# Performance work log

Hardware: AMD Instinct MI355X
Metric: run time of the kernel (lower is better)

The kernel has to match this reference:

```python
import jax, jax.numpy as jnp
import numpy as np

N = 100000
F_IN = 128
H = 128
E = 1600000
EP = 200000


def _gcn_conv(x, W, b, src, dst, n):
    # GCNConv (PyG default): add self-loops done by caller; symmetric norm; linear + scatter-add.
    xw = x @ W                                        # [n, H]
    deg = jax.ops.segment_sum(jnp.ones(src.shape[0], x.dtype), dst, num_segments=n)
    dinv = jnp.where(deg > 0, jax.lax.rsqrt(deg), 0.0)
    norm = dinv[src] * dinv[dst]                      # [E']
    msg = xw[src] * norm[:, None]                     # [E', H] gather
    out = jax.ops.segment_sum(msg, dst, num_segments=n)  # scatter-add
    return out + b


def setup_inputs() -> dict:
    key = jax.random.key(0)
    k = jax.random.split(key, 9)
    x = jax.random.normal(k[0], (N, F_IN), dtype=jnp.float32)
    edge_index = jax.random.randint(k[1], (2, E), 0, N, dtype=jnp.int64)
    dict_node = jax.random.randint(k[2], (N,), 0, N, dtype=jnp.int64)
    pos_edge_index = jax.random.randint(k[3], (2, EP), 0, N, dtype=jnp.int64)
    neg_edge_index = jax.random.randint(k[4], (2, EP), 0, N, dtype=jnp.int64)
    s1 = 1.0 / np.sqrt(F_IN)
    s2 = 1.0 / np.sqrt(H)
    W1 = jax.random.uniform(k[5], (F_IN, H), jnp.float32, -s1, s1)
    b1 = jnp.zeros((H,), jnp.float32)
    W2 = jax.random.uniform(k[6], (H, H), jnp.float32, -s2, s2)
    b2 = jnp.zeros((H,), jnp.float32)
    return {"x": x, "W1": W1, "b1": b1, "W2": W2, "b2": b2,
            "edge_index": edge_index, "dict_node": dict_node,
            "pos_edge_index": pos_edge_index, "neg_edge_index": neg_edge_index}


def reference(x, W1, b1, W2, b2, edge_index, dict_node, pos_edge_index, neg_edge_index):
    n = x.shape[0]
    # add self-loops once (both convs use the same edge_index)
    loop = jnp.arange(n, dtype=edge_index.dtype)
    src = jnp.concatenate([edge_index[0], loop])
    dst = jnp.concatenate([edge_index[1], loop])
    # encode (dropout p=0.01 is identity in eval mode)
    h = jax.nn.relu(_gcn_conv(x, W1, b1, src, dst, n))
    h = jax.nn.relu(_gcn_conv(h, W2, b2, src, dst, n))
    # global_mean_pool over dict_node segments (size = num_nodes)
    sums = jax.ops.segment_sum(h, dict_node, num_segments=n)
    cnt = jax.ops.segment_sum(jnp.ones((n,), h.dtype), dict_node, num_segments=n)
    z = sums / jnp.maximum(cnt, 1.0)[:, None]
    # decode: per-edge dot products over concatenated pos/neg edges
    ei = jnp.concatenate([pos_edge_index, neg_edge_index], axis=-1)
    logits = jnp.sum(z[ei[0]] * z[ei[1]], axis=-1)
    return logits
```

## Files before the change

### kernel.cpp

```cpp
#include <hip/hip_runtime.h>
#include <hip/hip_fp16.h>

#define HH 128
#define PCHUNK 16384


__global__ __launch_bounds__(256) void part_count_k(const int* __restrict__ key, int e,
                                                    int nbkt, int nblk,
                                                    int* __restrict__ gcnt,
                                                    int* __restrict__ blkoff) {
  __shared__ int h[512];
  for (int i = threadIdx.x; i < nbkt; i += 256) h[i] = 0;
  __syncthreads();
  int start = blockIdx.x * PCHUNK;
  int cnt = e - start; if (cnt > PCHUNK) cnt = PCHUNK;
  for (int i = threadIdx.x; i < cnt; i += 256)
    atomicAdd(&h[key[start + i] >> 8], 1);
  __syncthreads();
  for (int i = threadIdx.x; i < nbkt; i += 256) {
    int c = h[i];
    if (c) blkoff[(size_t)i * nblk + blockIdx.x] = atomicAdd(&gcnt[i], c);
  }
}

__global__ __launch_bounds__(512) void scan_bkt_k(const int* __restrict__ gcnt,
                                                  int* __restrict__ bktbase, int nbkt, int e) {
  __shared__ int sc[512];
  int tid = threadIdx.x;
  int v = (tid < nbkt) ? gcnt[tid] : 0;
  sc[tid] = v;
  __syncthreads();
  for (int off = 1; off < 512; off <<= 1) {
    int t = (tid >= off) ? sc[tid - off] : 0;
    __syncthreads();
    sc[tid] += t;
    __syncthreads();
  }
  if (tid < nbkt) bktbase[tid] = sc[tid] - v;
  if (tid == 0) bktbase[nbkt] = e;
}

__global__ __launch_bounds__(256) void part_scatter_k(const int* __restrict__ src,
                                                      const int* __restrict__ key, int e,
                                                      int nbkt, int nblk,
                                                      const int* __restrict__ bktbase,
                                                      const int* __restrict__ blkoff,
                                                      int2* __restrict__ part) {
  __shared__ int cur[512];
  for (int i = threadIdx.x; i < nbkt; i += 256)
    cur[i] = bktbase[i] + blkoff[(size_t)i * nblk + blockIdx.x];
  __syncthreads();
  int start = blockIdx.x * PCHUNK;
  int cnt = e - start; if (cnt > PCHUNK) cnt = PCHUNK;
  for (int i = threadIdx.x; i < cnt; i += 256) {
    int d = key[start + i], s = src[start + i];
    int pos = atomicAdd(&cur[d >> 8], 1);
    part[pos] = make_int2(s, d);
  }
}

__global__ __launch_bounds__(256) void part_scatter_idx_k(const int* __restrict__ key, int e,
                                                          int nbkt, int nblk,
                                                          const int* __restrict__ bktbase,
                                                          const int* __restrict__ blkoff,
                                                          int2* __restrict__ part) {
  __shared__ int cur[512];
  for (int i = threadIdx.x; i < nbkt; i += 256)
    cur[i] = bktbase[i] + blkoff[(size_t)i * nblk + blockIdx.x];
  __syncthreads();
  int start = blockIdx.x * PCHUNK;
  int cnt = e - start; if (cnt > PCHUNK) cnt = PCHUNK;
  for (int i = threadIdx.x; i < cnt; i += 256) {
    int d = key[start + i];
    int pos = atomicAdd(&cur[d >> 8], 1);
    part[pos] = make_int2(start + i, d);
  }
}

__global__ __launch_bounds__(256) void bucket_csr_k(const int2* __restrict__ part,
                                                    const int* __restrict__ bktbase,
                                                    int* __restrict__ rowptr,
                                                    float* __restrict__ dinv,
                                                    int* __restrict__ esrc,
                                                    int n, int e, int nbkt) {
  __shared__ int hist[256];
  __shared__ int sc[256];
  __shared__ int cur[256];
  int tid = threadIdx.x;
  int b = blockIdx.x;
  int dstbase = b << 8;
  int nloc = n - dstbase; if (nloc > 256) nloc = 256;
  int beg = bktbase[b], bend = bktbase[b + 1];

  hist[tid] = 0;
  __syncthreads();
  for (int j = beg + tid; j < bend; j += 256)
    atomicAdd(&hist[part[j].y & 255], 1);
  __syncthreads();
  int v = hist[tid];
  sc[tid] = v;
  __syncthreads();
  for (int off = 1; off < 256; off <<= 1) {
    int t = (tid >= off) ? sc[tid - off] : 0;
    __syncthreads();
    sc[tid] += t;
    __syncthreads();
  }
  int excl = sc[tid] - v;
  if (tid < nloc) {
    rowptr[dstbase + tid] = beg + excl;
    cur[tid] = beg + excl;
    if (dinv) dinv[dstbase + tid] = rsqrtf((float)v + 1.0f);
  }
  __syncthreads();
  for (int j = beg + tid; j < bend; j += 256) {
    int2 p = part[j];
    int pos = atomicAdd(&cur[p.y & 255], 1);
    esrc[pos] = p.x;
  }
  if (b == nbkt - 1 && tid == 0) rowptr[n] = e;
}

template <bool OUT16>
__global__ __launch_bounds__(256) void gemm128_v4(const float* __restrict__ A,
                                                  const float* __restrict__ W,
                                                  const float* __restrict__ dscale,
                                                  void* __restrict__ out, int n) {
  __shared__ float As[64][65];
  const int tid = threadIdx.x;
  const int rbase = blockIdx.x * 64;
  const int vrows = (n - rbase) < 64 ? (n - rbase) : 64;

  const int r = tid & 63;
  const int q = __builtin_amdgcn_readfirstlane(tid >> 6);
  const float* Wq = W + q * 32;

  float4 acc[8];
  #pragma unroll
  for (int c = 0; c < 8; ++c) acc[c] = make_float4(0.f, 0.f, 0.f, 0.f);

  #pragma unroll
  for (int ph = 0; ph < 2; ++ph) {
    if (ph) __syncthreads();
    #pragma unroll
    for (int j = 0; j < 4; ++j) {
      int f = tid + 256 * j;
      int rr = f >> 4, c4 = f & 15;
      float4 v = (rr < vrows)
          ? ((const float4*)(A + (size_t)(rbase + rr) * HH + ph * 64))[c4]
          : make_float4(0.f, 0.f, 0.f, 0.f);
      As[rr][c4 * 4 + 0] = v.x;
      As[rr][c4 * 4 + 1] = v.y;
      As[rr][c4 * 4 + 2] = v.z;
      As[rr][c4 * 4 + 3] = v.w;
    }
    __syncthreads();

    #pragma unroll 4
    for (int kk = 0; kk < 64; ++kk) {
      float a = As[r][kk];
      const float4* Wr = (const float4*)(Wq + (size_t)(ph * 64 + kk) * HH);
      #pragma unroll
      for (int c = 0; c < 8; ++c) {
        float4 w = Wr[c];
        acc[c].x += a * w.x; acc[c].y += a * w.y;
        acc[c].z += a * w.z; acc[c].w += a * w.w;
      }
    }
  }

  int row = rbase + r;
  if (row < n) {
    float s = dscale ? dscale[row] : 1.0f;
    if (OUT16) {
      uint2* o = (uint2*)((__half*)out + (size_t)row * HH) + q * 8;
      #pragma unroll
      for (int c = 0; c < 8; ++c) {
        __half2 h0 = __float22half2_rn(make_float2(acc[c].x * s, acc[c].y * s));
        __half2 h1 = __float22half2_rn(make_float2(acc[c].z * s, acc[c].w * s));
        uint2 u;
        u.x = *reinterpret_cast<unsigned*>(&h0);
        u.y = *reinterpret_cast<unsigned*>(&h1);
        o[c] = u;
      }
    } else {
      float4* o = (float4*)((float*)out + (size_t)row * HH + q * 32);
      #pragma unroll
      for (int c = 0; c < 8; ++c) {
        acc[c].x *= s; acc[c].y *= s; acc[c].z *= s; acc[c].w *= s;
        o[c] = acc[c];
      }
    }
  }
}

__global__ __launch_bounds__(256) void gather16_k(const __half* __restrict__ xw16,
                                                  const int* __restrict__ rowptr,
                                                  const int* __restrict__ esrc,
                                                  const float* __restrict__ dinv,
                                                  const float* __restrict__ bias,
                                                  float* __restrict__ h, int n) {
  int wid = (int)((blockIdx.x * (size_t)blockDim.x + threadIdx.x) >> 6);
  int lane = threadIdx.x & 63;
  if (wid >= n) return;
  int beg = rowptr[wid], end = rowptr[wid + 1];
  int half = lane >> 5, l32 = lane & 31;
  const uint2* base = (const uint2*)xw16 + l32;
  float4 acc = make_float4(0.f, 0.f, 0.f, 0.f);

  for (int j0 = beg; j0 < end; j0 += 64) {
    int myj = j0 + lane;
    int sv = (myj < end) ? esrc[myj] : 0;
    int cnt = end - j0; if (cnt > 64) cnt = 64;
    int k = 0;
    for (; k + 8 <= cnt; k += 8) {
      #pragma unroll
      for (int p = 0; p < 4; ++p) {
        int sa = __builtin_amdgcn_readlane(sv, k + 2 * p);
        int sb = __builtin_amdgcn_readlane(sv, k + 2 * p + 1);
        unsigned off = (unsigned)(half ? sb : sa) << 5;
        uint2 u = base[off];
        float2 f0 = __half22float2(*reinterpret_cast<__half2*>(&u.x));
        float2 f1 = __half22float2(*reinterpret_cast<__half2*>(&u.y));
        acc.x += f0.x; acc.y += f0.y; acc.z += f1.x; acc.w += f1.y;
      }
    }
    for (; k + 2 <= cnt; k += 2) {
      int sa = __builtin_amdgcn_readlane(sv, k);
      int sb = __builtin_amdgcn_readlane(sv, k + 1);
      unsigned off = (unsigned)(half ? sb : sa) << 5;
      uint2 u = base[off];
      float2 f0 = __half22float2(*reinterpret_cast<__half2*>(&u.x));
      float2 f1 = __half22float2(*reinterpret_cast<__half2*>(&u.y));
      acc.x += f0.x; acc.y += f0.y; acc.z += f1.x; acc.w += f1.y;
    }
    if (k < cnt) {
      int sa = __builtin_amdgcn_readlane(sv, k);
      if (half == 0) {
        uint2 u = base[(unsigned)sa << 5];
        float2 f0 = __half22float2(*reinterpret_cast<__half2*>(&u.x));
        float2 f1 = __half22float2(*reinterpret_cast<__half2*>(&u.y));
        acc.x += f0.x; acc.y += f0.y; acc.z += f1.x; acc.w += f1.y;
      }
    }
  }
  acc.x += __shfl_xor(acc.x, 32);
  acc.y += __shfl_xor(acc.y, 32);
  acc.z += __shfl_xor(acc.z, 32);
  acc.w += __shfl_xor(acc.w, 32);
  if (half == 0) {
    uint2 u = base[(unsigned)wid << 5];
    float2 s0 = __half22float2(*reinterpret_cast<__half2*>(&u.x));
    float2 s1 = __half22float2(*reinterpret_cast<__half2*>(&u.y));
    float di = dinv[wid];
    float4 bb = ((const float4*)bias)[l32];
    float4 o;
    o.x = fmaxf(bb.x + di * (acc.x + s0.x), 0.f);
    o.y = fmaxf(bb.y + di * (acc.y + s0.y), 0.f);
    o.z = fmaxf(bb.z + di * (acc.z + s1.x), 0.f);
    o.w = fmaxf(bb.w + di * (acc.w + s1.y), 0.f);
    ((float4*)h)[((size_t)wid << 5) + l32] = o;
  }
}

__global__ __launch_bounds__(256) void decode_fused3_k(const float* __restrict__ h2,
                                                       const int* __restrict__ rowptr,
                                                       const int* __restrict__ nodelist,
                                                       const int* __restrict__ pos,
                                                       const int* __restrict__ neg,
                                                       float* __restrict__ out, int ep) {
  int wv = (int)((blockIdx.x * (size_t)blockDim.x + threadIdx.x) >> 6);
  int lane = threadIdx.x & 63;
  int qq = lane >> 4, l16 = lane & 15;
  int e0 = wv * 2;
  if (e0 >= 2 * ep) return;
  int edge = e0 + (qq >> 1);
  int side = qq & 1;
  bool live = edge < 2 * ep;
  int eL = live ? edge : 2 * ep - 1;
  int node;
  if (eL < ep) node = side ? pos[ep + eL] : pos[eL];
  else { int t = eL - ep; node = side ? neg[ep + t] : neg[t]; }

  int beg = rowptr[node], end = rowptr[node + 1];
  const float4* h4 = (const float4*)h2;
  float4 a0 = make_float4(0.f, 0.f, 0.f, 0.f);
  float4 a1 = make_float4(0.f, 0.f, 0.f, 0.f);
  float4 c0 = make_float4(0.f, 0.f, 0.f, 0.f);
  float4 c1 = make_float4(0.f, 0.f, 0.f, 0.f);

  for (int j = beg; j < end; j += 2) {
    bool two = (j + 1) < end;
    int m0 = nodelist[j];
    int m1 = two ? nodelist[j + 1] : m0;
    const float4* r0 = h4 + ((size_t)m0 << 5);
    const float4* r1 = h4 + ((size_t)m1 << 5);
    float4 u0 = r0[l16], u1 = r0[l16 + 16];
    float4 v0 = r1[l16], v1 = r1[l16 + 16];
    a0.x += u0.x; a0.y += u0.y; a0.z += u0.z; a0.w += u0.w;
    a1.x += u1.x; a1.y += u1.y; a1.z += u1.z; a1.w += u1.w;
    if (two) {
      c0.x += v0.x; c0.y += v0.y; c0.z += v0.z; c0.w += v0.w;
      c1.x += v1.x; c1.y += v1.y; c1.z += v1.z; c1.w += v1.w;
    }
  }
  a0.x += c0.x; a0.y += c0.y; a0.z += c0.z; a0.w += c0.w;
  a1.x += c1.x; a1.y += c1.y; a1.z += c1.z; a1.w += c1.w;

  float inv = 1.0f / fmaxf((float)(end - beg), 1.0f);
  a0.x *= inv; a0.y *= inv; a0.z *= inv; a0.w *= inv;
  a1.x *= inv; a1.y *= inv; a1.z *= inv; a1.w *= inv;

  float4 b0, b1;
  b0.x = __shfl_xor(a0.x, 16); b0.y = __shfl_xor(a0.y, 16);
  b0.z = __shfl_xor(a0.z, 16); b0.w = __shfl_xor(a0.w, 16);
  b1.x = __shfl_xor(a1.x, 16); b1.y = __shfl_xor(a1.y, 16);
  b1.z = __shfl_xor(a1.z, 16); b1.w = __shfl_xor(a1.w, 16);
  float p = a0.x * b0.x + a0.y * b0.y + a0.z * b0.z + a0.w * b0.w
          + a1.x * b1.x + a1.y * b1.y + a1.z * b1.z + a1.w * b1.w;
  #pragma unroll
  for (int off = 8; off > 0; off >>= 1) p += __shfl_xor(p, off);
  if (live && side == 0 && l16 == 0) out[edge] = p;
}

__global__ void fill_deg_k(float* __restrict__ deg, int n) {
  int i = blockIdx.x * blockDim.x + threadIdx.x;
  if (i < n) deg[i] = 1.0f;
}
__global__ void accum_deg_k(const int* __restrict__ dst, float* __restrict__ deg, int e) {
  int i = blockIdx.x * blockDim.x + threadIdx.x;
  if (i < e) atomicAdd(&deg[dst[i]], 1.0f);
}
__global__ void dinv_k(float* __restrict__ deg, int n) {
  int i = blockIdx.x * blockDim.x + threadIdx.x;
  if (i < n) deg[i] = rsqrtf(deg[i]);
}
__global__ void init_h_k(const float* __restrict__ xw, const float* __restrict__ bias,
                         const float* __restrict__ dinv, float* __restrict__ h, int n) {
  int gid = blockIdx.x * blockDim.x + threadIdx.x;
  int node = gid >> 5, c4 = gid & 31;
  if (node >= n) return;
  float di = dinv[node];
  float nm = di * di;
  float4 v = ((const float4*)(xw + (size_t)node * HH))[c4];
  float4 b = ((const float4*)bias)[c4];
  ((float4*)(h + (size_t)node * HH))[c4] =
      make_float4(b.x + nm * v.x, b.y + nm * v.y, b.z + nm * v.z, b.w + nm * v.w);
}
__global__ void scatter_k(const float* __restrict__ xw, float* __restrict__ h,
                          const float* __restrict__ dinv, const int* __restrict__ src,
                          const int* __restrict__ dst, int e) {
  int gid = blockIdx.x * blockDim.x + threadIdx.x;
  int edge = gid >> 5, lane = gid & 31;
  if (edge >= e) return;
  int s = src[edge], d = dst[edge];
  float norm = dinv[s] * dinv[d];
  float4 v = ((const float4*)(xw + (size_t)s * HH))[lane];
  float* o = h + (size_t)d * HH + lane * 4;
  atomicAdd(o + 0, norm * v.x);
  atomicAdd(o + 1, norm * v.y);
  atomicAdd(o + 2, norm * v.z);
  atomicAdd(o + 3, norm * v.w);
}
__global__ void relu_k(float4* __restrict__ h, int n4) {
  int i = blockIdx.x * blockDim.x + threadIdx.x;
  if (i < n4) {
    float4 v = h[i];
    v.x = fmaxf(v.x, 0.f); v.y = fmaxf(v.y, 0.f);
    v.z = fmaxf(v.z, 0.f); v.w = fmaxf(v.w, 0.f);
    h[i] = v;
  }
}
__global__ void pool_accum_k(const float* __restrict__ h, const int* __restrict__ dict,
                             float* __restrict__ z, float* __restrict__ cnt, int n) {
  int gid = blockIdx.x * blockDim.x + threadIdx.x;
  int node = gid >> 5, lane = gid & 31;
  if (node >= n) return;
  int d = dict[node];
  float4 v = ((const float4*)(h + (size_t)node * HH))[lane];
  float* o = z + (size_t)d * HH + lane * 4;
  atomicAdd(o + 0, v.x); atomicAdd(o + 1, v.y);
  atomicAdd(o + 2, v.z); atomicAdd(o + 3, v.w);
  if (lane == 0) atomicAdd(&cnt[d], 1.0f);
}
__global__ void pool_div_k(float* __restrict__ z, const float* __restrict__ cnt, int n) {
  int gid = blockIdx.x * blockDim.x + threadIdx.x;
  int node = gid >> 5, lane = gid & 31;
  if (node >= n) return;
  float inv = 1.0f / fmaxf(cnt[node], 1.0f);
  float4* p = (float4*)(z + (size_t)node * HH) + lane;
  float4 v = *p;
  v.x *= inv; v.y *= inv; v.z *= inv; v.w *= inv;
  *p = v;
}
__global__ void decode_k(const float* __restrict__ z, const int* __restrict__ pos,
                         const int* __restrict__ neg, float* __restrict__ out, int ep) {
  int gid = blockIdx.x * blockDim.x + threadIdx.x;
  int edge = gid >> 5, lane = gid & 31;
  if (edge >= 2 * ep) return;
  int a, b;
  if (edge < ep) { a = pos[edge];      b = pos[ep + edge]; }
  else           { a = neg[edge - ep]; b = neg[edge]; }
  const float4* za = (const float4*)(z + (size_t)a * HH);
  const float4* zb = (const float4*)(z + (size_t)b * HH);
  float4 va = za[lane], vb = zb[lane];
  float dot = va.x * vb.x + va.y * vb.y + va.z * vb.z + va.w * vb.w;
  #pragma unroll
  for (int off = 16; off > 0; off >>= 1) dot += __shfl_xor(dot, off);
  if (lane == 0) out[edge] = dot;
}

extern "C" void kernel_launch(void* const* d_in, const int* in_sizes, int n_in,
                              void* d_out, int out_size, void* d_ws, size_t ws_size,
                              hipStream_t stream) {
  const float* x  = (const float*)d_in[0];
  const float* W1 = (const float*)d_in[1];
  const float* b1 = (const float*)d_in[2];
  const float* W2 = (const float*)d_in[3];
  const float* b2 = (const float*)d_in[4];
  const int* ei   = (const int*)d_in[5];
  const int* dict = (const int*)d_in[6];
  const int* pe   = (const int*)d_in[7];
  const int* ne   = (const int*)d_in[8];

  const int n  = in_sizes[0] / HH;
  const int e  = in_sizes[5] / 2;
  const int ep = in_sizes[7] / 2;
  const int* src = ei;
  const int* dst = ei + e;

  const size_t nf = (size_t)n * HH;
  const int nbkt  = (n + 255) >> 8;
  const int nblkE = (e + PCHUNK - 1) / PCHUNK;
  const int nblkN = (n + PCHUNK - 1) / PCHUNK;

  float*  p0     = (float*)d_ws;
  float*  bufF   = p0;
  __half* xw16   = (__half*)(p0 + nf);
  float*  dinv   = p0 + nf + nf / 2;
  int*    rowptr = (int*)(dinv + n);
  int*    tmp    = rowptr + (n + 1);
  int*    esrc   = tmp + n;
  int*    bsum   = esrc + e;
  int*    gcnt   = bsum + 256;
  int*    bktbase = gcnt + nbkt;
  size_t need = (nf + nf / 2 + n) * sizeof(float) +
                (size_t)(3 * n + 1 + e + 256 + 2 * nbkt + 1) * sizeof(int);

  int2* partE   = (int2*)bufF;
  int*  blkoffE = (int*)xw16;
  int2* partN   = (int2*)xw16;
  int*  blkoffN = (int*)(partN + n);

  const int nb    = (n + 255) / 256;
  const int nb32  = (int)(((size_t)n * 32 + 255) / 256);
  const int nb64  = (int)(((size_t)n * 64 + 255) / 256);
  const int gemb  = (n + 63) / 64;
  const int deb2  = (int)(((size_t)ep * 64 + 255) / 256);

  bool fast = (ws_size >= need) && (nbkt <= 512) &&
              ((size_t)nbkt * nblkE * 2 <= nf) && ((size_t)e * 2 <= nf);

  if (fast) {
    hipMemsetAsync(gcnt, 0, (size_t)nbkt * sizeof(int), stream);
    part_count_k<<<nblkE, 256, 0, stream>>>(dst, e, nbkt, nblkE, gcnt, blkoffE);
    scan_bkt_k<<<1, 512, 0, stream>>>(gcnt, bktbase, nbkt, e);
    part_scatter_k<<<nblkE, 256, 0, stream>>>(src, dst, e, nbkt, nblkE, bktbase, blkoffE, partE);
    bucket_csr_k<<<nbkt, 256, 0, stream>>>(partE, bktbase, rowptr, dinv, esrc, n, e, nbkt);

    gemm128_v4<true><<<gemb, 256, 0, stream>>>(x, W1, dinv, xw16, n);
    gather16_k<<<nb64, 256, 0, stream>>>(xw16, rowptr, esrc, dinv, b1, bufF, n);
    gemm128_v4<true><<<gemb, 256, 0, stream>>>(bufF, W2, dinv, xw16, n);
    gather16_k<<<nb64, 256, 0, stream>>>(xw16, rowptr, esrc, dinv, b2, bufF, n);

    hipMemsetAsync(gcnt, 0, (size_t)nbkt * sizeof(int), stream);
    part_count_k<<<nblkN, 256, 0, stream>>>(dict, n, nbkt, nblkN, gcnt, blkoffN);
    scan_bkt_k<<<1, 512, 0, stream>>>(gcnt, bktbase, nbkt, n);
    part_scatter_idx_k<<<nblkN, 256, 0, stream>>>(dict, n, nbkt, nblkN, bktbase, blkoffN, partN);
    bucket_csr_k<<<nbkt, 256, 0, stream>>>(partN, bktbase, rowptr, nullptr, esrc, n, n, nbkt);

    decode_fused3_k<<<deb2, 256, 0, stream>>>(bufF, rowptr, esrc, pe, ne, (float*)d_out, ep);
  } else {
    float* bufA  = (float*)d_ws;
    float* bufB  = bufA + nf;
    float* dinv2 = bufB + nf;
    float* cnt   = dinv2 + n;
    fill_deg_k<<<nb, 256, 0, stream>>>(dinv2, n);
    accum_deg_k<<<(e + 255) / 256, 256, 0, stream>>>(dst, dinv2, e);
    dinv_k<<<nb, 256, 0, stream>>>(dinv2, n);

    gemm128_v4<false><<<gemb, 256, 0, stream>>>(x, W1, nullptr, bufA, n);
    init_h_k<<<nb32, 256, 0, stream>>>(bufA, b1, dinv2, bufB, n);
    scatter_k<<<(int)(((size_t)e * 32 + 255) / 256), 256, 0, stream>>>(bufA, bufB, dinv2, src, dst, e);
    relu_k<<<nb32, 256, 0, stream>>>((float4*)bufB, n * 32);

    gemm128_v4<false><<<gemb, 256, 0, stream>>>(bufB, W2, nullptr, bufA, n);
    init_h_k<<<nb32, 256, 0, stream>>>(bufA, b2, dinv2, bufB, n);
    scatter_k<<<(int)(((size_t)e * 32 + 255) / 256), 256, 0, stream>>>(bufA, bufB, dinv2, src, dst, e);
    relu_k<<<nb32, 256, 0, stream>>>((float4*)bufB, n * 32);

    hipMemsetAsync(bufA, 0, nf * sizeof(float), stream);
    hipMemsetAsync(cnt, 0, (size_t)n * sizeof(float), stream);
    pool_accum_k<<<nb32, 256, 0, stream>>>(bufB, dict, bufA, cnt, n);
    pool_div_k<<<nb32, 256, 0, stream>>>(bufA, cnt, n);
    decode_k<<<(int)(((size_t)2 * ep * 32 + 255) / 256), 256, 0, stream>>>(
        bufA, pe, ne, (float*)d_out, ep);
  }
}
```

Measured before the change: 406.9 us.

## Pack partition entries into one int and store second-layer output in fp16

The bucket partition now packs the source index and the low 8 bits of the destination into a single 32-bit int instead of an int2. This halves the partition write and read traffic in the scatter and CSR-build kernels. The second GCN gather now writes its output in fp16, and the decode kernel reads fp16 rows, halving h2 write and gather traffic. The trade-offs are reduced precision in the final embeddings and a new limit of n < 2^23 on the fast path.

```diff
diff --git a/kernel.cpp b/kernel.cpp
--- a/kernel.cpp
+++ b/kernel.cpp
@@ -45,7 +45,7 @@
                                                       int nbkt, int nblk,
                                                       const int* __restrict__ bktbase,
                                                       const int* __restrict__ blkoff,
-                                                      int2* __restrict__ part) {
+                                                      int* __restrict__ part) {
   __shared__ int cur[512];
   for (int i = threadIdx.x; i < nbkt; i += 256)
     cur[i] = bktbase[i] + blkoff[(size_t)i * nblk + blockIdx.x];
@@ -55,7 +55,7 @@
   for (int i = threadIdx.x; i < cnt; i += 256) {
     int d = key[start + i], s = src[start + i];
     int pos = atomicAdd(&cur[d >> 8], 1);
-    part[pos] = make_int2(s, d);
+    part[pos] = (s << 8) | (d & 255);
   }
 }
 
@@ -63,7 +63,7 @@
                                                           int nbkt, int nblk,
                                                           const int* __restrict__ bktbase,
                                                           const int* __restrict__ blkoff,
-                                                          int2* __restrict__ part) {
+                                                          int* __restrict__ part) {
   __shared__ int cur[512];
   for (int i = threadIdx.x; i < nbkt; i += 256)
     cur[i] = bktbase[i] + blkoff[(size_t)i * nblk + blockIdx.x];
@@ -73,11 +73,11 @@
   for (int i = threadIdx.x; i < cnt; i += 256) {
     int d = key[start + i];
     int pos = atomicAdd(&cur[d >> 8], 1);
-    part[pos] = make_int2(start + i, d);
-  }
-}
-
-__global__ __launch_bounds__(256) void bucket_csr_k(const int2* __restrict__ part,
+    part[pos] = ((start + i) << 8) | (d & 255);
+  }
+}
+
+__global__ __launch_bounds__(256) void bucket_csr_k(const int* __restrict__ part,
                                                     const int* __restrict__ bktbase,
                                                     int* __restrict__ rowptr,
                                                     float* __restrict__ dinv,
@@ -95,7 +95,7 @@
   hist[tid] = 0;
   __syncthreads();
   for (int j = beg + tid; j < bend; j += 256)
-    atomicAdd(&hist[part[j].y & 255], 1);
+    atomicAdd(&hist[part[j] & 255], 1);
   __syncthreads();
   int v = hist[tid];
   sc[tid] = v;
@@ -114,9 +114,9 @@
   }
   __syncthreads();
   for (int j = beg + tid; j < bend; j += 256) {
-    int2 p = part[j];
-    int pos = atomicAdd(&cur[p.y & 255], 1);
-    esrc[pos] = p.x;
+    int p = part[j];
+    int pos = atomicAdd(&cur[p & 255], 1);
+    esrc[pos] = p >> 8;
   }
   if (b == nbkt - 1 && tid == 0) rowptr[n] = e;
 }
@@ -194,12 +194,13 @@
   }
 }
 
+template <bool HOUT16>
 __global__ __launch_bounds__(256) void gather16_k(const __half* __restrict__ xw16,
                                                   const int* __restrict__ rowptr,
                                                   const int* __restrict__ esrc,
                                                   const float* __restrict__ dinv,
                                                   const float* __restrict__ bias,
-                                                  float* __restrict__ h, int n) {
+                                                  void* __restrict__ h, int n) {
   int wid = (int)((blockIdx.x * (size_t)blockDim.x + threadIdx.x) >> 6);
   int lane = threadIdx.x & 63;
   if (wid >= n) return;
@@ -259,11 +260,20 @@
     o.y = fmaxf(bb.y + di * (acc.y + s0.y), 0.f);
     o.z = fmaxf(bb.z + di * (acc.z + s1.x), 0.f);
     o.w = fmaxf(bb.w + di * (acc.w + s1.y), 0.f);
-    ((float4*)h)[((size_t)wid << 5) + l32] = o;
-  }
-}
-
-__global__ __launch_bounds__(256) void decode_fused3_k(const float* __restrict__ h2,
+    if (HOUT16) {
+      __half2 p0 = __float22half2_rn(make_float2(o.x, o.y));
+      __half2 p1 = __float22half2_rn(make_float2(o.z, o.w));
+      uint2 w;
+      w.x = *reinterpret_cast<unsigned*>(&p0);
+      w.y = *reinterpret_cast<unsigned*>(&p1);
+      ((uint2*)h)[((size_t)wid << 5) + l32] = w;
+    } else {
+      ((float4*)h)[((size_t)wid << 5) + l32] = o;
+    }
+  }
+}
+
+__global__ __launch_bounds__(256) void decode_fused4_k(const __half* __restrict__ h2,
                                                        const int* __restrict__ rowptr,
                                                        const int* __restrict__ nodelist,
                                                        const int* __restrict__ pos,
@@ -283,7 +293,7 @@
   else { int t = eL - ep; node = side ? neg[ep + t] : neg[t]; }
 
   int beg = rowptr[node], end = rowptr[node + 1];
-  const float4* h4 = (const float4*)h2;
+  const uint2* h4 = (const uint2*)h2;
   float4 a0 = make_float4(0.f, 0.f, 0.f, 0.f);
   float4 a1 = make_float4(0.f, 0.f, 0.f, 0.f);
   float4 c0 = make_float4(0.f, 0.f, 0.f, 0.f);
@@ -293,15 +303,20 @@
     bool two = (j + 1) < end;
     int m0 = nodelist[j];
     int m1 = two ? nodelist[j + 1] : m0;
-    const float4* r0 = h4 + ((size_t)m0 << 5);
-    const float4* r1 = h4 + ((size_t)m1 << 5);
-    float4 u0 = r0[l16], u1 = r0[l16 + 16];
-    float4 v0 = r1[l16], v1 = r1[l16 + 16];
-    a0.x += u0.x; a0.y += u0.y; a0.z += u0.z; a0.w += u0.w;
-    a1.x += u1.x; a1.y += u1.y; a1.z += u1.z; a1.w += u1.w;
+    const uint2* r0 = h4 + ((size_t)m0 << 5);
+    const uint2* r1 = h4 + ((size_t)m1 << 5);
+    uint2 u0 = r0[l16], u1 = r0[l16 + 16];
+    uint2 v0 = r1[l16], v1 = r1[l16 + 16];
+    float2 f;
+    f = __half22float2(*reinterpret_cast<__half2*>(&u0.x)); a0.x += f.x; a0.y += f.y;
+    f = __half22float2(*reinterpret_cast<__half2*>(&u0.y)); a0.z += f.x; a0.w += f.y;
+    f = __half22float2(*reinterpret_cast<__half2*>(&u1.x)); a1.x += f.x; a1.y += f.y;
+    f = __half22float2(*reinterpret_cast<__half2*>(&u1.y)); a1.z += f.x; a1.w += f.y;
     if (two) {
-      c0.x += v0.x; c0.y += v0.y; c0.z += v0.z; c0.w += v0.w;
-      c1.x += v1.x; c1.y += v1.y; c1.z += v1.z; c1.w += v1.w;
+      f = __half22float2(*reinterpret_cast<__half2*>(&v0.x)); c0.x += f.x; c0.y += f.y;
+      f = __half22float2(*reinterpret_cast<__half2*>(&v0.y)); c0.z += f.x; c0.w += f.y;
+      f = __half22float2(*reinterpret_cast<__half2*>(&v1.x)); c1.x += f.x; c1.y += f.y;
+      f = __half22float2(*reinterpret_cast<__half2*>(&v1.y)); c1.z += f.x; c1.w += f.y;
     }
   }
   a0.x += c0.x; a0.y += c0.y; a0.z += c0.z; a0.w += c0.w;
@@ -447,10 +462,10 @@
   size_t need = (nf + nf / 2 + n) * sizeof(float) +
                 (size_t)(3 * n + 1 + e + 256 + 2 * nbkt + 1) * sizeof(int);
 
-  int2* partE   = (int2*)bufF;
-  int*  blkoffE = (int*)xw16;
-  int2* partN   = (int2*)xw16;
-  int*  blkoffN = (int*)(partN + n);
+  int* partE   = (int*)bufF;
+  int* blkoffE = (int*)xw16;
+  int* partN   = (int*)xw16;
+  int* blkoffN = partN + n;
 
   const int nb    = (n + 255) / 256;
   const int nb32  = (int)(((size_t)n * 32 + 255) / 256);
@@ -458,8 +473,8 @@
   const int gemb  = (n + 63) / 64;
   const int deb2  = (int)(((size_t)ep * 64 + 255) / 256);
 
-  bool fast = (ws_size >= need) && (nbkt <= 512) &&
-              ((size_t)nbkt * nblkE * 2 <= nf) && ((size_t)e * 2 <= nf);
+  bool fast = (ws_size >= need) && (nbkt <= 512) && (n < (1 << 23)) &&
+              ((size_t)e <= nf) && ((size_t)nbkt * nblkE * 2 <= nf);
 
   if (fast) {
     hipMemsetAsync(gcnt, 0, (size_t)nbkt * sizeof(int), stream);
@@ -469,9 +484,10 @@
     bucket_csr_k<<<nbkt, 256, 0, stream>>>(partE, bktbase, rowptr, dinv, esrc, n, e, nbkt);
 
     gemm128_v4<true><<<gemb, 256, 0, stream>>>(x, W1, dinv, xw16, n);
-    gather16_k<<<nb64, 256, 0, stream>>>(xw16, rowptr, esrc, dinv, b1, bufF, n);
+    gather16_k<false><<<nb64, 256, 0, stream>>>(xw16, rowptr, esrc, dinv, b1, bufF, n);
     gemm128_v4<true><<<gemb, 256, 0, stream>>>(bufF, W2, dinv, xw16, n);
-    gather16_k<<<nb64, 256, 0, stream>>>(xw16, rowptr, esrc, dinv, b2, bufF, n);
+    __half* h2_16 = (__half*)bufF;
+    gather16_k<true><<<nb64, 256, 0, stream>>>(xw16, rowptr, esrc, dinv, b2, h2_16, n);
 
     hipMemsetAsync(gcnt, 0, (size_t)nbkt * sizeof(int), stream);
     part_count_k<<<nblkN, 256, 0, stream>>>(dict, n, nbkt, nblkN, gcnt, blkoffN);
@@ -479,7 +495,7 @@
     part_scatter_idx_k<<<nblkN, 256, 0, stream>>>(dict, n, nbkt, nblkN, bktbase, blkoffN, partN);
     bucket_csr_k<<<nbkt, 256, 0, stream>>>(partN, bktbase, rowptr, nullptr, esrc, n, n, nbkt);
 
-    decode_fused3_k<<<deb2, 256, 0, stream>>>(bufF, rowptr, esrc, pe, ne, (float*)d_out, ep);
+    decode_fused4_k<<<deb2, 256, 0, stream>>>(h2_16, rowptr, esrc, pe, ne, (float*)d_out, ep);
   } else {
     float* bufA  = (float*)d_ws;
     float* bufB  = bufA + nf;
```

Result: faster. 398.1 us (-2.1%).
